# Kernel optimization log

Hardware: AMD Instinct MI355X
Metric: run time of the kernel (lower is better)

Reference implementation:

```python
import jax, jax.numpy as jnp
import numpy as np

WS = 7        # window size (cubic)
SHIFT = 3     # shift size (cubic)
NH = 6        # num heads
EPS = 1e-5


def _layernorm(x, g, b):
    m = x.mean(-1, keepdims=True)
    v = ((x - m) ** 2).mean(-1, keepdims=True)
    return (x - m) / jnp.sqrt(v + EPS) * g + b


def _win_partition(x, ws):
    # (B,H,W,T,C) -> (B*nW, ws^3, C)
    B, H, W, T, C = x.shape
    x = x.reshape(B, H // ws, ws, W // ws, ws, T // ws, ws, C)
    return x.transpose(0, 1, 3, 5, 2, 4, 6, 7).reshape(-1, ws * ws * ws, C)


def _win_reverse(w, ws, B, H, W, T):
    # (B*nW, ws^3, C) -> (B,H,W,T,C)
    C = w.shape[-1]
    x = w.reshape(B, H // ws, W // ws, T // ws, ws, ws, ws, C)
    return x.transpose(0, 1, 4, 2, 5, 3, 6, 7).reshape(B, H, W, T, C)


def _rel_index(ws):
    # 3D relative position index, (N, N) int, N = ws^3 (torch.meshgrid default 'ij')
    coords = np.stack(np.meshgrid(np.arange(ws), np.arange(ws), np.arange(ws), indexing='ij'))
    cf = coords.reshape(3, -1)
    rel = (cf[:, :, None] - cf[:, None, :]).transpose(1, 2, 0)
    rel[:, :, 0] += ws - 1
    rel[:, :, 1] += ws - 1
    rel[:, :, 2] += ws - 1
    rel[:, :, 0] *= (2 * ws - 1) ** 2
    rel[:, :, 1] *= (2 * ws - 1)
    return rel.sum(-1)


def _compute_mask(Hp, Wp, Tp, ws, shift):
    img = np.zeros((1, Hp, Wp, Tp, 1), np.float32)
    cnt = 0
    sl = (slice(0, -ws), slice(-ws, -shift), slice(-shift, None))
    for h in sl:
        for w in sl:
            for t in sl:
                img[:, h, w, t, :] = cnt
                cnt += 1
    mw = np.asarray(_win_partition(jnp.asarray(img), ws)).reshape(-1, ws ** 3)  # (nW, N)
    am = mw[:, None, :] - mw[:, :, None]
    return jnp.asarray(np.where(am != 0, -100.0, 0.0).astype(np.float32))


def setup_inputs() -> dict:
    key = jax.random.key(0)
    ks = jax.random.split(key, 10)
    B, Hd, Wd, Td, C = 2, 28, 28, 28, 192
    L = Hd * Wd * Td
    Ch = int(C * 4.0)
    s = 0.02
    inp = {
        'x': jax.random.normal(ks[0], (B, L, C), jnp.float32),
        'mask': _compute_mask(Hd, Wd, Td, WS, SHIFT),
        'gamma1': jnp.ones((C,), jnp.float32),
        'beta1': jnp.zeros((C,), jnp.float32),
        'qkv_w': jax.random.normal(ks[1], (3 * C, C), jnp.float32) * s,
        'qkv_b': jnp.zeros((3 * C,), jnp.float32),
        'rpb_table': jax.random.normal(ks[2], ((2 * WS - 1) ** 3, NH), jnp.float32) * s,
        'proj_w': jax.random.normal(ks[3], (C, C), jnp.float32) * s,
        'proj_b': jnp.zeros((C,), jnp.float32),
        'gamma2': jnp.ones((C,), jnp.float32),
        'beta2': jnp.zeros((C,), jnp.float32),
        'fc1_w': jax.random.normal(ks[4], (Ch, C), jnp.float32) * s,
        'fc1_b': jnp.zeros((Ch,), jnp.float32),
        'fc2_w': jax.random.normal(ks[5], (C, Ch), jnp.float32) * s,
        'fc2_b': jnp.zeros((C,), jnp.float32),
        'H': Hd, 'W': Wd, 'T': Td,
    }
    return inp


def reference(x, mask, gamma1, beta1, qkv_w, qkv_b, rpb_table, proj_w, proj_b,
              gamma2, beta2, fc1_w, fc1_b, fc2_w, fc2_b, H, W, T):
    B, L, C = x.shape
    hd = C // NH
    scale = hd ** -0.5
    shortcut = x

    h1 = _layernorm(x, gamma1, beta1).reshape(B, H, W, T, C)
    # H,W,T are multiples of WS -> no padding; cyclic shift for SW-MSA
    shifted = jnp.roll(h1, (-SHIFT, -SHIFT, -SHIFT), axis=(1, 2, 3))
    xw = _win_partition(shifted, WS)            # (B*nW, N, C)
    Bn, N, _ = xw.shape

    qkv = (xw @ qkv_w.T + qkv_b).reshape(Bn, N, 3, NH, hd).transpose(2, 0, 3, 1, 4)
    q, k, v = qkv[0] * scale, qkv[1], qkv[2]     # (Bn, NH, N, hd)
    attn = jnp.einsum('bhnd,bhmd->bhnm', q, k)   # (Bn, NH, N, N)

    idx = _rel_index(WS)
    bias = rpb_table[idx.reshape(-1)].reshape(N, N, NH).transpose(2, 0, 1)
    attn = attn + bias[None]

    nW = mask.shape[0]
    attn = attn.reshape(Bn // nW, nW, NH, N, N) + mask[None, :, None]
    attn = jax.nn.softmax(attn.reshape(Bn, NH, N, N), axis=-1)

    out = jnp.einsum('bhnm,bhmd->bhnd', attn, v).transpose(0, 2, 1, 3).reshape(Bn, N, C)
    out = out @ proj_w.T + proj_b

    shifted = _win_reverse(out, WS, B, H, W, T)
    xr = jnp.roll(shifted, (SHIFT, SHIFT, SHIFT), axis=(1, 2, 3)).reshape(B, L, C)

    x = shortcut + xr
    h2 = _layernorm(x, gamma2, beta2)
    m = jax.nn.gelu(h2 @ fc1_w.T + fc1_b, approximate=False)
    return x + (m @ fc2_w.T + fc2_b)
```

## Files before the change

### kernel.cpp

```cpp
#include <hip/hip_runtime.h>
#include <hip/hip_bf16.h>

typedef unsigned short u16;
typedef unsigned int u32;
typedef __attribute__((ext_vector_type(8))) short s16x8;
typedef __attribute__((ext_vector_type(4))) float f32x4;

__device__ __forceinline__ u16 f2bf(float f) {
    union { float f; u32 u; } x; x.f = f;
    u32 r = x.u + 0x7fffu + ((x.u >> 16) & 1u);
    return (u16)(r >> 16);
}
__device__ __forceinline__ float bflo(u32 v) {
    union { u32 u; float f; } x; x.u = v << 16; return x.f;
}
__device__ __forceinline__ float bfhi(u32 v) {
    union { u32 u; float f; } x; x.u = v & 0xffff0000u; return x.f;
}
__device__ __forceinline__ u32 cvt_pk_bf16(float a, float b) {
    u32 r;
    asm("v_cvt_pk_bf16_f32 %0, %1, %2" : "=v"(r) : "v"(a), "v"(b));
    return r;
}
__device__ __forceinline__ void gl2lds(const u16* g, u16* l) {
    __builtin_amdgcn_global_load_lds(
        (const __attribute__((address_space(1))) unsigned int*)g,
        (__attribute__((address_space(3))) unsigned int*)l, 16, 0, 0);
}

#define L_TOK 21952
#define C_DIM 192
#define LOG2E 1.4426950408889634f
#define Q2SCALE 0.2550565444463649f
#define BT_STR 352

__global__ __launch_bounds__(256) void cvt_k(const float* __restrict__ s0,
                                             const float* __restrict__ s1,
                                             const float* __restrict__ s2,
                                             const float* __restrict__ s3,
                                             u16* __restrict__ dst)
{
    int i = blockIdx.x * 256 + threadIdx.x;
    float v;
    if (i < 110592) v = s0[i];
    else if (i < 147456) v = s1[i - 110592];
    else if (i < 294912) v = s2[i - 147456];
    else v = s3[i - 294912];
    dst[i] = f2bf(v);
}

__global__ __launch_bounds__(256) void bias48_k(const float* __restrict__ rpb,
                                                u16* __restrict__ biasT)
{
    const int gid = blockIdx.x * 256 + threadIdx.x;
    const int z = gid / 30976;
    const int rem = gid - z * 30976;
    const int m = rem / 88;
    const int n0 = (rem - m * 88) * 4;
    const int hh = z >> 3, wt = z & 7;

    u16 v[4];
    if (m <= 342) {
        const int hm = m / 49, r2 = m - hm * 49, wm = r2 / 7, tm = r2 - wm * 7;
        const int rm = ((wt & 4) ? (hm < 4 ? 1 : 2) : 0) * 9
                     + ((wt & 2) ? (wm < 4 ? 1 : 2) : 0) * 3
                     + ((wt & 1) ? (tm < 4 ? 1 : 2) : 0);
        #pragma unroll
        for (int j = 0; j < 4; j++) {
            const int n = n0 + j;
            float b = -100000.0f;
            if (n <= 342) {
                int hq = n / 49, r1 = n - hq * 49, wq = r1 / 7, tq = r1 - wq * 7;
                int idx = ((hq - hm + 6) * 13 + (wq - wm + 6)) * 13 + (tq - tm + 6);
                b = rpb[idx * 6 + hh];
                int rq = ((wt & 4) ? (hq < 4 ? 1 : 2) : 0) * 9
                       + ((wt & 2) ? (wq < 4 ? 1 : 2) : 0) * 3
                       + ((wt & 1) ? (tq < 4 ? 1 : 2) : 0);
                if (rq != rm) b -= 100.0f;
                b *= LOG2E;
            }
            v[j] = f2bf(b);
        }
    } else {
        const u16 neg = f2bf(-100000.0f);
        v[0] = neg; v[1] = neg; v[2] = neg; v[3] = neg;
    }
    u32 lo = (u32)v[0] | ((u32)v[1] << 16);
    u32 hi = (u32)v[2] | ((u32)v[3] << 16);
    *(uint2*)&biasT[((size_t)z * 352 + m) * BT_STR + n0] = (uint2){lo, hi};
}

template<int MODE>
__global__ __launch_bounds__(256) void ln_k(const float* __restrict__ in,
                                            const float* __restrict__ g,
                                            const float* __restrict__ b,
                                            u16* __restrict__ out)
{
    const int lane = threadIdx.x & 63, wv = threadIdx.x >> 6;
    const int tok = blockIdx.x * 4 + wv;
    size_t base = (size_t)tok * C_DIM;
    float x0 = in[base + lane];
    float x1 = in[base + 64 + lane];
    float x2 = in[base + 128 + lane];
    float s = x0 + x1 + x2;
    float sq = x0 * x0 + x1 * x1 + x2 * x2;
    #pragma unroll
    for (int off = 32; off > 0; off >>= 1) {
        s += __shfl_xor(s, off, 64);
        sq += __shfl_xor(sq, off, 64);
    }
    const float mean = s * (1.0f / 192.0f);
    float var = sq * (1.0f / 192.0f) - mean * mean;
    var = fmaxf(var, 0.0f);
    const float rstd = rsqrtf(var + 1e-5f);

    size_t obase;
    if (MODE == 0) {
        int bi = tok / L_TOK;
        int l = tok - bi * L_TOK;
        int h = l / 784;
        int rm = l - h * 784;
        int w = rm / 28;
        int t = rm - w * 28;
        int hs = h + 25; if (hs >= 28) hs -= 28;
        int ws = w + 25; if (ws >= 28) ws -= 28;
        int ts = t + 25; if (ts >= 28) ts -= 28;
        int win = ((bi * 4 + hs / 7) * 4 + ws / 7) * 4 + ts / 7;
        int n = (hs % 7) * 49 + (ws % 7) * 7 + (ts % 7);
        obase = ((size_t)win * 343 + n) * C_DIM;
    } else {
        obase = base;
    }
    #pragma unroll
    for (int i = 0; i < 3; i++) {
        int c = lane + i * 64;
        float xv = (i == 0) ? x0 : (i == 1) ? x1 : x2;
        float y = (xv - mean) * rstd * g[c] + b[c];
        out[obase + c] = f2bf(y);
    }
}

template<int K, int EPI>
__global__ __launch_bounds__(256) void gemm_k(const u16* __restrict__ A,
                                              const u16* __restrict__ W,
                                              const float* __restrict__ bias,
                                              void* __restrict__ outp,
                                              const void* __restrict__ resp,
                                              int Ncols)
{
    constexpr int NC = K / 64;
    __shared__ __align__(16) u16 As[2][2 * 64 * 32 * 2];
    __shared__ __align__(16) u16 Bs[2][2 * 64 * 32];
    const int t = threadIdx.x;
    const int bm = blockIdx.y;
    const int n0 = blockIdx.x * 64;
    const int lane = t & 63, wv = t >> 6;
    const int wm = (wv >> 1) * 64, wn = (wv & 1) * 32;
    const int r16 = lane & 15, quad = lane >> 4;

    f32x4 acc[4][2];
    #pragma unroll
    for (int i = 0; i < 4; i++)
        #pragma unroll
        for (int j = 0; j < 2; j++) acc[i][j] = (f32x4){0.f, 0.f, 0.f, 0.f};

    const int ar = t >> 2, ac = (t & 3) * 8;
    const size_t abase = (size_t)bm * 128 * K;

    auto STAGE = [&](int c, int b) {
        #pragma unroll
        for (int kt = 0; kt < 2; kt++) {
            const int k0 = c * 64 + kt * 32;
            gl2lds(&A[abase + (size_t)ar * K + k0 + ac], &As[b][kt * 4096 + 8 * t]);
            gl2lds(&A[abase + (size_t)(ar + 64) * K + k0 + ac], &As[b][kt * 4096 + 2048 + 8 * t]);
            gl2lds(&W[(size_t)(n0 + ar) * K + k0 + ac], &Bs[b][kt * 2048 + 8 * t]);
        }
    };

    STAGE(0, 0);
    __syncthreads();
    for (int c = 0; c < NC; ++c) {
        const int cur = c & 1;
        if (c + 1 < NC) STAGE(c + 1, cur ^ 1);
        #pragma unroll
        for (int kt = 0; kt < 2; kt++) {
            s16x8 af[4], bf[2];
            #pragma unroll
            for (int fm = 0; fm < 4; fm++)
                af[fm] = *(const s16x8*)&As[cur][kt * 4096 + (wm + fm * 16 + r16) * 32 + quad * 8];
            #pragma unroll
            for (int fn = 0; fn < 2; fn++)
                bf[fn] = *(const s16x8*)&Bs[cur][kt * 2048 + (wn + fn * 16 + r16) * 32 + quad * 8];
            #pragma unroll
            for (int fm = 0; fm < 4; fm++)
                #pragma unroll
                for (int fn = 0; fn < 2; fn++)
                    acc[fm][fn] = __builtin_amdgcn_mfma_f32_16x16x32_bf16(af[fm], bf[fn], acc[fm][fn], 0, 0, 0);
        }
        __syncthreads();
    }

    #pragma unroll
    for (int fm = 0; fm < 4; fm++) {
        #pragma unroll
        for (int fn = 0; fn < 2; fn++) {
            #pragma unroll
            for (int r = 0; r < 4; r++) {
                const int grow = bm * 128 + wm + fm * 16 + quad * 4 + r;
                const int gcol = n0 + wn + fn * 16 + r16;
                float v = acc[fm][fn][r] + bias[gcol];
                if (EPI == 0) {
                    if (gcol < 192) v *= Q2SCALE;
                    ((u16*)outp)[(size_t)grow * Ncols + gcol] = f2bf(v);
                } else if (EPI == 1) {
                    v = 0.5f * v * (1.0f + erff(v * 0.70710678118654752f));
                    ((u16*)outp)[(size_t)grow * Ncols + gcol] = f2bf(v);
                } else if (EPI == 2) {
                    size_t o = (size_t)grow * C_DIM + gcol;
                    ((float*)outp)[o] = v + ((const float*)resp)[o];
                } else {
                    int win = grow / 343, n = grow - win * 343;
                    int bi = win >> 6, wi = win & 63;
                    int hw = wi >> 4, ww = (wi >> 2) & 3, tw = wi & 3;
                    int ph = n / 49, rem = n - ph * 49;
                    int pw = rem / 7, pt = rem - pw * 7;
                    int h = hw * 7 + ph + 3; if (h >= 28) h -= 28;
                    int w = ww * 7 + pw + 3; if (w >= 28) w -= 28;
                    int tt = tw * 7 + pt + 3; if (tt >= 28) tt -= 28;
                    int l = (h * 28 + w) * 28 + tt;
                    size_t o = ((size_t)bi * L_TOK + l) * C_DIM + gcol;
                    ((float*)outp)[o] = v + ((const float*)resp)[o];
                }
            }
        }
    }
}

__global__ __launch_bounds__(256, 3) void attn_k(const u16* __restrict__ qkv,
                                                 const u16* __restrict__ biasAll,
                                                 u16* __restrict__ out)
{
    __shared__ __align__(16) u16 Ks[352 * 32];
    __shared__ __align__(16) u16 Vt[32 * 360];
    __shared__ __align__(16) u16 Pb[4][16 * 40];

    const int hh = blockIdx.x;
    const int win = blockIdx.y;
    const int wi = win & 63;
    const int t = threadIdx.x, lane = t & 63, wv = t >> 6;
    const int r16 = lane & 15, quad = lane >> 4;
    const size_t qbase = (size_t)win * 343 * 576 + hh * 32;

    for (int j = t; j < 343 * 4; j += 256) {
        int m = j >> 2, ch = j & 3;
        *(uint4*)&Ks[m * 32 + ch * 8] = *(const uint4*)&qkv[qbase + (size_t)m * 576 + 192 + ch * 8];
    }
    if (t < 36) {
        int m = 343 + (t >> 2), ch = t & 3;
        *(uint4*)&Ks[m * 32 + ch * 8] = (uint4){0u, 0u, 0u, 0u};
    }
    for (int i = t; i < 343 * 16; i += 256) {
        int m = i >> 4, d2 = (i & 15) * 2;
        int pm = (m & ~31) + 2 * (m & 15) + ((m >> 4) & 1);
        u32 w2 = *(const u32*)&qkv[qbase + (size_t)m * 576 + 384 + d2];
        Vt[d2 * 360 + pm] = (u16)(w2 & 0xffffu);
        Vt[(d2 + 1) * 360 + pm] = (u16)(w2 >> 16);
    }
    for (int i = t; i < 32 * 9; i += 256) {
        int d = i / 9, m = 343 + i % 9;
        int pm = (m & ~31) + 2 * (m & 15) + ((m >> 4) & 1);
        Vt[d * 360 + pm] = 0;
    }
    __syncthreads();

    const int wt = (((wi >> 4) == 3) ? 4 : 0) | ((((wi >> 2) & 3) == 3) ? 2 : 0)
                 | (((wi & 3) == 3) ? 1 : 0);
    const u16* biashT = biasAll + (size_t)(hh * 8 + wt) * 352 * BT_STR;

    s16x8 onesb;
    #pragma unroll
    for (int j = 0; j < 8; j++) onesb[j] = (short)0x3f80;

    for (int qt = 0; qt < 6; qt++) {
        const int row0 = qt * 64 + wv * 16;
        if (row0 > 342) continue;
        int qrow = row0 + r16; if (qrow > 342) qrow = 342;
        s16x8 qa = *(const s16x8*)&qkv[qbase + (size_t)qrow * 576 + quad * 8];

        const int n0 = row0 + quad * 4;

        f32x4 sacc[22];
        #pragma unroll
        for (int fn = 0; fn < 22; fn++) {
            const int col = fn * 16 + r16;
            uint2 bv = *(const uint2*)&biashT[(size_t)col * BT_STR + n0];
            sacc[fn][0] = bflo(bv.x);
            sacc[fn][1] = bfhi(bv.x);
            sacc[fn][2] = bflo(bv.y);
            sacc[fn][3] = bfhi(bv.y);
        }
        #pragma unroll
        for (int fn = 0; fn < 22; fn++) {
            s16x8 kb = *(const s16x8*)&Ks[(fn * 16 + r16) * 32 + quad * 8];
            sacc[fn] = __builtin_amdgcn_mfma_f32_16x16x32_bf16(qa, kb, sacc[fn], 0, 0, 0);
        }

        #pragma unroll
        for (int fn = 0; fn < 22; fn++) {
            #pragma unroll
            for (int r = 0; r < 4; r++)
                sacc[fn][r] = exp2f(fminf(sacc[fn][r], 42.0f));
        }

        u16* pw = &Pb[wv][0];
        u32* pw32 = (u32*)pw;
        f32x4 oacc0 = (f32x4){0.f, 0.f, 0.f, 0.f};
        f32x4 oacc1 = (f32x4){0.f, 0.f, 0.f, 0.f};
        f32x4 osum  = (f32x4){0.f, 0.f, 0.f, 0.f};
        #pragma unroll
        for (int c = 0; c < 11; c++) {
            asm volatile("s_waitcnt lgkmcnt(0)" ::: "memory");
            #pragma unroll
            for (int r = 0; r < 4; r++)
                pw32[(quad * 4 + r) * 20 + r16] = cvt_pk_bf16(sacc[2 * c][r], sacc[2 * c + 1][r]);
            asm volatile("s_waitcnt lgkmcnt(0)" ::: "memory");
            s16x8 pa = *(const s16x8*)&pw[r16 * 40 + quad * 8];
            s16x8 vb0 = *(const s16x8*)&Vt[r16 * 360 + c * 32 + quad * 8];
            s16x8 vb1 = *(const s16x8*)&Vt[(16 + r16) * 360 + c * 32 + quad * 8];
            oacc0 = __builtin_amdgcn_mfma_f32_16x16x32_bf16(pa, vb0, oacc0, 0, 0, 0);
            oacc1 = __builtin_amdgcn_mfma_f32_16x16x32_bf16(pa, vb1, oacc1, 0, 0, 0);
            osum  = __builtin_amdgcn_mfma_f32_16x16x32_bf16(pa, onesb, osum, 0, 0, 0);
        }

        #pragma unroll
        for (int r = 0; r < 4; r++) {
            const int n = n0 + r;
            if (n < 343) {
                const float rs = osum[r];
                const float inv = rs > 0.0f ? 1.0f / rs : 0.0f;
                size_t o = ((size_t)win * 343 + n) * C_DIM + hh * 32;
                out[o + r16] = f2bf(oacc0[r] * inv);
                out[o + 16 + r16] = f2bf(oacc1[r] * inv);
            }
        }
    }
}

extern "C" void kernel_launch(void* const* d_in, const int* in_sizes, int n_in,
                              void* d_out, int out_size, void* d_ws, size_t ws_size,
                              hipStream_t stream)
{
    const float* x      = (const float*)d_in[0];
    const float* g1     = (const float*)d_in[2];
    const float* b1     = (const float*)d_in[3];
    const float* qkv_w  = (const float*)d_in[4];
    const float* qkv_b  = (const float*)d_in[5];
    const float* rpb    = (const float*)d_in[6];
    const float* proj_w = (const float*)d_in[7];
    const float* proj_b = (const float*)d_in[8];
    const float* g2     = (const float*)d_in[9];
    const float* b2     = (const float*)d_in[10];
    const float* fc1_w  = (const float*)d_in[11];
    const float* fc1_b  = (const float*)d_in[12];
    const float* fc2_w  = (const float*)d_in[13];
    const float* fc2_b  = (const float*)d_in[14];

    char* ws = (char*)d_ws;
    u16* xw        = (u16*)(ws + 0);
    u16* biasT     = (u16*)(ws + 0);
    u16* qkv       = (u16*)(ws + 16861184);
    u16* a1        = (u16*)(ws + 0);
    u16* attn_out  = (u16*)(ws + 67444736);
    u16* h2        = attn_out;
    float* x2      = (float*)(ws + 84305920);
    u16* wbf       = (u16*)(ws + 118028288);
    u16* qkv_wb = wbf;
    u16* proj_wb = wbf + 110592;
    u16* fc1_wb = wbf + 147456;
    u16* fc2_wb = wbf + 294912;

    cvt_k<<<dim3(1728), 256, 0, stream>>>(qkv_w, proj_w, fc1_w, fc2_w, wbf);
    ln_k<0><<<dim3(10976), 256, 0, stream>>>(x, g1, b1, xw);
    gemm_k<192, 0><<<dim3(9, 343), 256, 0, stream>>>(xw, qkv_wb, qkv_b, qkv, nullptr, 576);
    bias48_k<<<dim3(5808), 256, 0, stream>>>(rpb, biasT);
    attn_k<<<dim3(6, 128), 256, 0, stream>>>(qkv, biasT, attn_out);
    gemm_k<192, 3><<<dim3(3, 343), 256, 0, stream>>>(attn_out, proj_wb, proj_b, x2, x, 192);
    ln_k<1><<<dim3(10976), 256, 0, stream>>>(x2, g2, b2, h2);
    gemm_k<192, 1><<<dim3(12, 343), 256, 0, stream>>>(h2, fc1_wb, fc1_b, a1, nullptr, 768);
    gemm_k<768, 2><<<dim3(3, 343), 256, 0, stream>>>(a1, fc2_wb, fc2_b, d_out, x2, 192);
}
```

Measured before the change: 353.0 us.

## Keep full-K A tile resident in LDS and loop over multiple N tiles

Adds a K=192 GEMM kernel that loads the whole 128x192 A tile into LDS once and then iterates over several 64-column output tiles, reloading only the weight tile between them. It is used for the QKV, proj and FC1 GEMMs, which cuts redundant re-reads of the activation matrix across column blocks. The epilogue is factored into a shared helper that hoists the per-row address calculation, including the window-reverse index math, out of the column loop. The trade-off is a larger LDS footprint (about 72KB) that may lower occupancy, and fewer, longer blocks with less overlap between loading and compute.

```diff
diff --git a/kernel.cpp b/kernel.cpp
--- a/kernel.cpp
+++ b/kernel.cpp
@@ -140,6 +140,119 @@
     }
 }
 
+template<int EPI>
+__device__ __forceinline__ void gemm_epi(f32x4 acc[4][2], int bm, int n0,
+                                         int wm, int wn, int r16, int quad,
+                                         const float* __restrict__ bias,
+                                         void* __restrict__ outp,
+                                         const void* __restrict__ resp,
+                                         int Ncols)
+{
+    #pragma unroll
+    for (int fm = 0; fm < 4; fm++) {
+        #pragma unroll
+        for (int r = 0; r < 4; r++) {
+            const int grow = bm * 128 + wm + fm * 16 + quad * 4 + r;
+            size_t rowbase;
+            if (EPI == 3) {
+                int win = grow / 343, n = grow - win * 343;
+                int bi = win >> 6, wi = win & 63;
+                int hw = wi >> 4, ww = (wi >> 2) & 3, tw = wi & 3;
+                int ph = n / 49, rem = n - ph * 49;
+                int pw = rem / 7, pt = rem - pw * 7;
+                int h = hw * 7 + ph + 3; if (h >= 28) h -= 28;
+                int w = ww * 7 + pw + 3; if (w >= 28) w -= 28;
+                int tt = tw * 7 + pt + 3; if (tt >= 28) tt -= 28;
+                int l = (h * 28 + w) * 28 + tt;
+                rowbase = ((size_t)bi * L_TOK + l) * C_DIM;
+            } else {
+                rowbase = (size_t)grow * ((EPI == 2) ? C_DIM : Ncols);
+            }
+            #pragma unroll
+            for (int fn = 0; fn < 2; fn++) {
+                const int gcol = n0 + wn + fn * 16 + r16;
+                float v = acc[fm][fn][r] + bias[gcol];
+                if (EPI == 0) {
+                    if (gcol < 192) v *= Q2SCALE;
+                    ((u16*)outp)[rowbase + gcol] = f2bf(v);
+                } else if (EPI == 1) {
+                    v = 0.5f * v * (1.0f + erff(v * 0.70710678118654752f));
+                    ((u16*)outp)[rowbase + gcol] = f2bf(v);
+                } else {
+                    size_t o = rowbase + gcol;
+                    ((float*)outp)[o] = v + ((const float*)resp)[o];
+                }
+            }
+        }
+    }
+}
+
+template<int PER, int EPI>
+__global__ __launch_bounds__(256) void gemm_ar_k(const u16* __restrict__ A,
+                                                 const u16* __restrict__ W,
+                                                 const float* __restrict__ bias,
+                                                 void* __restrict__ outp,
+                                                 const void* __restrict__ resp,
+                                                 int Ncols)
+{
+    constexpr int K = 192;
+    __shared__ __align__(16) u16 As[6 * 128 * 32];
+    __shared__ __align__(16) u16 Bs[6 * 64 * 32];
+    const int t = threadIdx.x;
+    const int bm = blockIdx.y;
+    const int lane = t & 63, wv = t >> 6;
+    const int wm = (wv >> 1) * 64, wn = (wv & 1) * 32;
+    const int r16 = lane & 15, quad = lane >> 4;
+    const int ar = t >> 2, ac = (t & 3) * 8;
+    const size_t abase = (size_t)bm * 128 * K;
+    const int n0b = blockIdx.x * (PER * 64);
+
+    #pragma unroll
+    for (int kt = 0; kt < 6; kt++) {
+        gl2lds(&A[abase + (size_t)ar * K + kt * 32 + ac], &As[kt * 4096 + 8 * t]);
+        gl2lds(&A[abase + (size_t)(ar + 64) * K + kt * 32 + ac], &As[kt * 4096 + 2048 + 8 * t]);
+    }
+    #pragma unroll
+    for (int kt = 0; kt < 6; kt++)
+        gl2lds(&W[(size_t)(n0b + ar) * K + kt * 32 + ac], &Bs[kt * 2048 + 8 * t]);
+    __syncthreads();
+
+    #pragma unroll
+    for (int p = 0; p < PER; ++p) {
+        const int n0 = n0b + p * 64;
+        f32x4 acc[4][2];
+        #pragma unroll
+        for (int i = 0; i < 4; i++)
+            #pragma unroll
+            for (int j = 0; j < 2; j++) acc[i][j] = (f32x4){0.f, 0.f, 0.f, 0.f};
+
+        #pragma unroll
+        for (int kt = 0; kt < 6; kt++) {
+            s16x8 af[4], bf[2];
+            #pragma unroll
+            for (int fm = 0; fm < 4; fm++)
+                af[fm] = *(const s16x8*)&As[kt * 4096 + (wm + fm * 16 + r16) * 32 + quad * 8];
+            #pragma unroll
+            for (int fn = 0; fn < 2; fn++)
+                bf[fn] = *(const s16x8*)&Bs[kt * 2048 + (wn + fn * 16 + r16) * 32 + quad * 8];
+            #pragma unroll
+            for (int fm = 0; fm < 4; fm++)
+                #pragma unroll
+                for (int fn = 0; fn < 2; fn++)
+                    acc[fm][fn] = __builtin_amdgcn_mfma_f32_16x16x32_bf16(af[fm], bf[fn], acc[fm][fn], 0, 0, 0);
+        }
+
+        if (p + 1 < PER) {
+            __syncthreads();
+            #pragma unroll
+            for (int kt = 0; kt < 6; kt++)
+                gl2lds(&W[(size_t)(n0 + 64 + ar) * K + kt * 32 + ac], &Bs[kt * 2048 + 8 * t]);
+        }
+        gemm_epi<EPI>(acc, bm, n0, wm, wn, r16, quad, bias, outp, resp, Ncols);
+        if (p + 1 < PER) __syncthreads();
+    }
+}
+
 template<int K, int EPI>
 __global__ __launch_bounds__(256) void gemm_k(const u16* __restrict__ A,
                                               const u16* __restrict__ W,
@@ -200,40 +313,7 @@
         __syncthreads();
     }
 
-    #pragma unroll
-    for (int fm = 0; fm < 4; fm++) {
-        #pragma unroll
-        for (int fn = 0; fn < 2; fn++) {
-            #pragma unroll
-            for (int r = 0; r < 4; r++) {
-                const int grow = bm * 128 + wm + fm * 16 + quad * 4 + r;
-                const int gcol = n0 + wn + fn * 16 + r16;
-                float v = acc[fm][fn][r] + bias[gcol];
-                if (EPI == 0) {
-                    if (gcol < 192) v *= Q2SCALE;
-                    ((u16*)outp)[(size_t)grow * Ncols + gcol] = f2bf(v);
-                } else if (EPI == 1) {
-                    v = 0.5f * v * (1.0f + erff(v * 0.70710678118654752f));
-                    ((u16*)outp)[(size_t)grow * Ncols + gcol] = f2bf(v);
-                } else if (EPI == 2) {
-                    size_t o = (size_t)grow * C_DIM + gcol;
-                    ((float*)outp)[o] = v + ((const float*)resp)[o];
-                } else {
-                    int win = grow / 343, n = grow - win * 343;
-                    int bi = win >> 6, wi = win & 63;
-                    int hw = wi >> 4, ww = (wi >> 2) & 3, tw = wi & 3;
-                    int ph = n / 49, rem = n - ph * 49;
-                    int pw = rem / 7, pt = rem - pw * 7;
-                    int h = hw * 7 + ph + 3; if (h >= 28) h -= 28;
-                    int w = ww * 7 + pw + 3; if (w >= 28) w -= 28;
-                    int tt = tw * 7 + pt + 3; if (tt >= 28) tt -= 28;
-                    int l = (h * 28 + w) * 28 + tt;
-                    size_t o = ((size_t)bi * L_TOK + l) * C_DIM + gcol;
-                    ((float*)outp)[o] = v + ((const float*)resp)[o];
-                }
-            }
-        }
-    }
+    gemm_epi<EPI>(acc, bm, n0, wm, wn, r16, quad, bias, outp, resp, Ncols);
 }
 
 __global__ __launch_bounds__(256, 3) void attn_k(const u16* __restrict__ qkv,
@@ -381,11 +461,11 @@
 
     cvt_k<<<dim3(1728), 256, 0, stream>>>(qkv_w, proj_w, fc1_w, fc2_w, wbf);
     ln_k<0><<<dim3(10976), 256, 0, stream>>>(x, g1, b1, xw);
-    gemm_k<192, 0><<<dim3(9, 343), 256, 0, stream>>>(xw, qkv_wb, qkv_b, qkv, nullptr, 576);
+    gemm_ar_k<3, 0><<<dim3(3, 343), 256, 0, stream>>>(xw, qkv_wb, qkv_b, qkv, nullptr, 576);
     bias48_k<<<dim3(5808), 256, 0, stream>>>(rpb, biasT);
     attn_k<<<dim3(6, 128), 256, 0, stream>>>(qkv, biasT, attn_out);
-    gemm_k<192, 3><<<dim3(3, 343), 256, 0, stream>>>(attn_out, proj_wb, proj_b, x2, x, 192);
+    gemm_ar_k<1, 3><<<dim3(3, 343), 256, 0, stream>>>(attn_out, proj_wb, proj_b, x2, x, 192);
     ln_k<1><<<dim3(10976), 256, 0, stream>>>(x2, g2, b2, h2);
-    gemm_k<192, 1><<<dim3(12, 343), 256, 0, stream>>>(h2, fc1_wb, fc1_b, a1, nullptr, 768);
+    gemm_ar_k<4, 1><<<dim3(3, 343), 256, 0, stream>>>(h2, fc1_wb, fc1_b, a1, nullptr, 768);
     gemm_k<768, 2><<<dim3(3, 343), 256, 0, stream>>>(a1, fc2_wb, fc2_b, d_out, x2, 192);
 }
```

Result: slower. 375.8 us (+6.5%).
